# Performance work log

Measured on AMD Instinct MI355X. Metric: run time of the kernel, lower is better.

The kernel has to match this reference:

```python
import jax, jax.numpy as jnp
import numpy as np

B, S, D, H = 4, 2048, 1024, 16
DH = D // H          # per-head attention size (attention_size // n_heads)
F = 4 * D            # FFN hidden
EPS = 1e-5


def _layer_norm(x, g, b):
    m = jnp.mean(x, axis=-1, keepdims=True)
    v = jnp.mean(jnp.square(x - m), axis=-1, keepdims=True)
    return (x - m) * jax.lax.rsqrt(v + EPS) * g + b


def setup_inputs() -> dict:
    key = jax.random.key(0)
    ks = jax.random.split(key, 12)
    s = 0.02
    x = jax.random.normal(ks[0], (B, S, D), dtype=jnp.float32)
    # causal mask: True = masked (strict upper triangle)
    mask = jnp.broadcast_to(jnp.triu(jnp.ones((S, S), dtype=bool), k=1), (B, S, S))
    wq = jax.random.normal(ks[1], (H, D, DH), dtype=jnp.float32) * s
    wk = jax.random.normal(ks[2], (H, D, DH), dtype=jnp.float32) * s
    wv = jax.random.normal(ks[3], (H, D, DH), dtype=jnp.float32) * s
    wo = jax.random.normal(ks[4], (D, D), dtype=jnp.float32) * s   # attention_size -> embedding_dim
    w1 = jax.random.normal(ks[5], (D, F), dtype=jnp.float32) * s
    b1 = jax.random.normal(ks[6], (F,), dtype=jnp.float32) * s
    w2 = jax.random.normal(ks[7], (F, D), dtype=jnp.float32) * s
    b2 = jax.random.normal(ks[8], (D,), dtype=jnp.float32) * s
    ln1_g = jnp.ones((D,), jnp.float32) + jax.random.normal(ks[9], (D,), jnp.float32) * s
    ln1_b = jax.random.normal(ks[10], (D,), jnp.float32) * s
    ln2_g = jnp.ones((D,), jnp.float32) + jax.random.normal(ks[11], (D,), jnp.float32) * s
    ln2_b = jnp.zeros((D,), jnp.float32)
    return {"x": x, "mask": mask, "wq": wq, "wk": wk, "wv": wv, "wo": wo,
            "w1": w1, "b1": b1, "w2": w2, "b2": b2,
            "ln1_g": ln1_g, "ln1_b": ln1_b, "ln2_g": ln2_g, "ln2_b": ln2_b}


def reference(x, mask, wq, wk, wv, wo, w1, b1, w2, b2, ln1_g, ln1_b, ln2_g, ln2_b):
    # --- self-attention block (pre-norm, residual) ---
    h = _layer_norm(x, ln1_g, ln1_b)                       # [B,S,D]
    q = jnp.einsum('bsd,hde->bhse', h, wq)                 # [B,H,S,DH]
    k = jnp.einsum('bsd,hde->bhse', h, wk)
    v = jnp.einsum('bsd,hde->bhse', h, wv)
    scores = jnp.einsum('bhse,bhte->bhst', q, k)           # [B,H,S,S]
    # faithful to source: mask-fill with -inf, THEN divide by sqrt(head_dim)
    scores = jnp.where(mask[:, None, :, :], -jnp.inf, scores) / jnp.sqrt(jnp.float32(DH))
    p = jax.nn.softmax(scores, axis=-1)
    attn = jnp.einsum('bhst,bhte->bhse', p, v)             # [B,H,S,DH]
    concat = attn.transpose(0, 2, 1, 3).reshape(B, S, D)   # heads concatenated on feature dim
    x = x + concat @ wo
    # --- feed-forward block ---
    h2 = _layer_norm(x, ln2_g, ln2_b)
    ff = jax.nn.gelu(h2 @ w1 + b1, approximate=False) @ w2 + b2
    return x + ff
```

## Files before the change

kernel.cpp:

```cpp
#include <hip/hip_runtime.h>
#include <hip/hip_bf16.h>
#include <math.h>


#define Bz 4
#define Sz 2048
#define Dz 1024
#define Hz 16
#define DHz 64
#define Fz 4096
#define Mz 8192

typedef float f32x4 __attribute__((ext_vector_type(4)));
typedef __bf16 bf16x8 __attribute__((ext_vector_type(8)));
typedef __bf16 bf16x4 __attribute__((ext_vector_type(4)));
typedef short s16x4 __attribute__((ext_vector_type(4)));

#define GLOAD_LDS16(g, l)                                                                   \
  __builtin_amdgcn_global_load_lds((const __attribute__((address_space(1))) unsigned int*)(g), \
                                   (__attribute__((address_space(3))) unsigned int*)(l), 16, 0, 0)

static __device__ __forceinline__ unsigned short f2bu(float f) {
  unsigned int u = __float_as_uint(f);
  u += 0x7fffu + ((u >> 16) & 1u);
  return (unsigned short)(u >> 16);
}

static __device__ __forceinline__ f32x4 mfma32(bf16x8 a, bf16x8 b, f32x4 c) {
  return __builtin_amdgcn_mfma_f32_16x16x32_bf16(a, b, c, 0, 0, 0);
}
static __device__ __forceinline__ f32x4 mfma16(s16x4 a, s16x4 b, f32x4 c) {
#if __has_builtin(__builtin_amdgcn_mfma_f32_16x16x16bf16_1k)
  return __builtin_amdgcn_mfma_f32_16x16x16bf16_1k(a, b, c, 0, 0, 0);
#else
  asm("v_mfma_f32_16x16x16_bf16 %0, %1, %2, %0" : "+v"(c) : "v"(a), "v"(b));
  return c;
#endif
}

template <int OFF>
static __device__ __forceinline__ s16x4 tr16(unsigned addr) {
  s16x4 r;
  asm volatile("ds_read_b64_tr_b16 %0, %1 offset:%2" : "=v"(r) : "v"(addr), "i"(OFF));
  return r;
}


__global__ __launch_bounds__(256) void pack_qkv(
    const float* __restrict__ wq, const float* __restrict__ wk, const float* __restrict__ wv,
    unsigned short* __restrict__ outW)
{
  __shared__ float tile[64][65];
  const int blk = blockIdx.x;
  const int dc = blk & 15;
  const int h  = (blk >> 4) & 15;
  const int p  = blk >> 8;
  const float* w = p == 0 ? wq : (p == 1 ? wk : wv);
  const int tid = threadIdx.x;
#pragma unroll
  for (int i = 0; i < 4; ++i) {
    int idx = i * 256 + tid;
    int dl = idx >> 4;
    int e0 = (idx & 15) * 4;
    const float4 v = *(const float4*)&w[(size_t)(h * 1024 + dc * 64 + dl) * 64 + e0];
    tile[dl][e0 + 0] = v.x; tile[dl][e0 + 1] = v.y;
    tile[dl][e0 + 2] = v.z; tile[dl][e0 + 3] = v.w;
  }
  __syncthreads();
#pragma unroll
  for (int i = 0; i < 4; ++i) {
    int idx = i * 256 + tid;
    int e = idx >> 4;
    int d0 = (idx & 15) * 4;
    ushort4 o;
    o.x = f2bu(tile[d0 + 0][e]); o.y = f2bu(tile[d0 + 1][e]);
    o.z = f2bu(tile[d0 + 2][e]); o.w = f2bu(tile[d0 + 3][e]);
    *(ushort4*)&outW[(size_t)(p * 1024 + h * 64 + e) * 1024 + dc * 64 + d0] = o;
  }
}

__global__ __launch_bounds__(256) void transpose_f32_to_bf16(
    const float* __restrict__ in, unsigned short* __restrict__ out, int R, int C)
{
  __shared__ float tile[32][33];
  int c0 = blockIdx.x * 32, r0 = blockIdx.y * 32;
  int x = threadIdx.x, y = threadIdx.y;
#pragma unroll
  for (int i = 0; i < 32; i += 8)
    tile[y + i][x] = in[(size_t)(r0 + y + i) * C + c0 + x];
  __syncthreads();
#pragma unroll
  for (int i = 0; i < 32; i += 8)
    out[(size_t)(c0 + y + i) * R + r0 + x] = f2bu(tile[x][y + i]);
}


__global__ __launch_bounds__(256) void ln_kernel(
    const float* __restrict__ x, const float* __restrict__ gamma, const float* __restrict__ beta,
    unsigned short* __restrict__ outH)
{
  const int row = blockIdx.x;
  const int tid = threadIdx.x;
  const float4 v = ((const float4*)(x + (size_t)row * Dz))[tid];
  float s = v.x + v.y + v.z + v.w;
  float s2 = v.x * v.x + v.y * v.y + v.z * v.z + v.w * v.w;
#pragma unroll
  for (int o = 32; o > 0; o >>= 1) {
    s += __shfl_xor(s, o);
    s2 += __shfl_xor(s2, o);
  }
  __shared__ float ss[4], ss2[4];
  if ((tid & 63) == 0) { ss[tid >> 6] = s; ss2[tid >> 6] = s2; }
  __syncthreads();
  s = ss[0] + ss[1] + ss[2] + ss[3];
  s2 = ss2[0] + ss2[1] + ss2[2] + ss2[3];
  const float mean = s * (1.0f / Dz);
  const float rstd = rsqrtf(s2 * (1.0f / Dz) - mean * mean + 1e-5f);
  const float4 g4 = ((const float4*)gamma)[tid];
  const float4 b4 = ((const float4*)beta)[tid];
  ushort4 o;
  o.x = f2bu((v.x - mean) * rstd * g4.x + b4.x);
  o.y = f2bu((v.y - mean) * rstd * g4.y + b4.y);
  o.z = f2bu((v.z - mean) * rstd * g4.z + b4.z);
  o.w = f2bu((v.w - mean) * rstd * g4.w + b4.w);
  ((ushort4*)(outH + (size_t)row * Dz))[tid] = o;
}


enum { EPI_BF16 = 0, EPI_GELU_BF16 = 1, EPI_RES_F32 = 2, EPI_BIAS_RES_F32 = 3 };

template <int BM, int EPI>
__global__ __launch_bounds__(512, 2) void gemm256(
    const unsigned short* __restrict__ A,
    const unsigned short* __restrict__ BT,
    int M, int N, int K,
    const float* bias, const float* resid,
    unsigned short* outb, float* outf)
{
  constexpr int BN = 256, BK = 64;
  constexpr int DEPTH = (BM == 128) ? 3 : 2;
  constexpr int ACH = (BM * BK * 2) / (512 * 16);
  constexpr int BCH = (BN * BK * 2) / (512 * 16);
  constexpr int MREP = BM / 32;
  __shared__ unsigned short As[DEPTH][BM * BK];
  __shared__ unsigned short Bs[DEPTH][BN * BK];

  const int tid = threadIdx.x;
  const int lane = tid & 63;
  const int wid = tid >> 6;
  const int wr = wid >> 2;
  const int wc = wid & 3;
  const int rsel = lane & 15;
  const int kgrp = lane >> 4;

  const int nwg = gridDim.x;
  const int bid = blockIdx.x;
  const int id2 = (bid & 7) * (nwg >> 3) + (bid >> 3);
  const int nbx = N / BN;
  const int n0 = (id2 % nbx) * BN;
  const int m0 = (id2 / nbx) * BM;

  f32x4 acc[MREP][4] = {};

  auto issue = [&](int kt, int b) {
#pragma unroll
    for (int r = 0; r < ACH; ++r) {
      int gc = r * 512 + tid;
      int row = gc >> 3;
      int kcs = (gc & 7) ^ (row & 7);
      GLOAD_LDS16(A + (size_t)(m0 + row) * K + kt * BK + kcs * 8, &As[b][gc * 8]);
    }
#pragma unroll
    for (int r = 0; r < BCH; ++r) {
      int gc = r * 512 + tid;
      int row = gc >> 3;
      int kcs = (gc & 7) ^ (row & 7);
      GLOAD_LDS16(BT + (size_t)(n0 + row) * K + kt * BK + kcs * 8, &Bs[b][gc * 8]);
    }
  };

  const int T = K >> 6;
#pragma unroll
  for (int d = 0; d < DEPTH - 1; ++d) issue(d, d);

  for (int t = 0; t < T; ++t) {
    const int b = t % DEPTH;
    if (t + DEPTH - 1 < T) issue(t + DEPTH - 1, (t + DEPTH - 1) % DEPTH);
    int rem = T - 1 - t;
    if (rem > DEPTH - 1) rem = DEPTH - 1;
    if constexpr (DEPTH == 3) {
      if (rem == 2)      asm volatile("s_waitcnt vmcnt(12)" ::: "memory");
      else if (rem == 1) asm volatile("s_waitcnt vmcnt(6)" ::: "memory");
      else               asm volatile("s_waitcnt vmcnt(0)" ::: "memory");
    } else {
      if (rem == 1) asm volatile("s_waitcnt vmcnt(8)" ::: "memory");
      else          asm volatile("s_waitcnt vmcnt(0)" ::: "memory");
    }
    __builtin_amdgcn_sched_barrier(0);
    __builtin_amdgcn_s_barrier();
    __builtin_amdgcn_sched_barrier(0);

    const unsigned short* Ab = As[b];
    const unsigned short* Bb = Bs[b];
    __builtin_amdgcn_s_setprio(1);
#pragma unroll
    for (int kk = 0; kk < 2; ++kk) {
      bf16x8 bfr[4], af[MREP];
#pragma unroll
      for (int nf = 0; nf < 4; ++nf) {
        int br = wc * 64 + nf * 16 + rsel;
        bfr[nf] = *(const bf16x8*)&Bb[br * BK + (((kk * 4 + kgrp) ^ (br & 7)) * 8)];
      }
#pragma unroll
      for (int mf = 0; mf < MREP; ++mf) {
        int ar = wr * (BM / 2) + mf * 16 + rsel;
        af[mf] = *(const bf16x8*)&Ab[ar * BK + (((kk * 4 + kgrp) ^ (ar & 7)) * 8)];
      }
#pragma unroll
      for (int mf = 0; mf < MREP; ++mf)
#pragma unroll
        for (int nf = 0; nf < 4; ++nf)
          acc[mf][nf] = mfma32(af[mf], bfr[nf], acc[mf][nf]);
    }
    __builtin_amdgcn_s_setprio(0);
    __builtin_amdgcn_sched_barrier(0);
    __builtin_amdgcn_s_barrier();
  }

#pragma unroll
  for (int mf = 0; mf < MREP; ++mf) {
#pragma unroll
    for (int nf = 0; nf < 4; ++nf) {
      const int n = n0 + wc * 64 + nf * 16 + rsel;
#pragma unroll
      for (int j = 0; j < 4; ++j) {
        const int m = m0 + wr * (BM / 2) + mf * 16 + kgrp * 4 + j;
        const size_t idx = (size_t)m * N + n;
        float v = acc[mf][nf][j];
        if constexpr (EPI == EPI_BF16) {
          outb[idx] = f2bu(v);
        } else if constexpr (EPI == EPI_GELU_BF16) {
          v += bias[n];
          v = 0.5f * v * (1.0f + erff(v * 0.70710678118654752f));
          outb[idx] = f2bu(v);
        } else if constexpr (EPI == EPI_RES_F32) {
          outf[idx] = v + resid[idx];
        } else {
          outf[idx] = v + bias[n] + resid[idx];
        }
      }
    }
  }
}


__global__ __launch_bounds__(256, 4) void attn_kernel(
    const unsigned short* __restrict__ QKV,
    unsigned short* __restrict__ outA)
{
  __shared__ unsigned short Kt[64 * 64];
  __shared__ unsigned short Vs[64 * 64];
  const int pi = blockIdx.x;
  const int hh = blockIdx.y;
  const int bb = blockIdx.z;
  const int tid = threadIdx.x;
  const int lane = tid & 63;
  const int w = tid >> 6;
  const int rsel = lane & 15;
  const int kgrp = lane >> 4;
  const int qt[2] = {pi, 31 - pi};

  bf16x8 qf0[2], qf1[2];
  int qg[2];
#pragma unroll
  for (int s = 0; s < 2; ++s) {
    qg[s] = qt[s] * 64 + w * 16 + rsel;
    const size_t rowQ = (size_t)(bb * Sz + qg[s]) * 3072 + hh * 64;
    qf0[s] = *(const bf16x8*)&QKV[rowQ + kgrp * 8];
    qf1[s] = *(const bf16x8*)&QKV[rowQ + 32 + kgrp * 8];
  }

  f32x4 accO[2][4] = {};
  float mr[2] = {-INFINITY, -INFINITY};
  float lr[2] = {0.0f, 0.0f};

  auto vs3 = (__attribute__((address_space(3))) unsigned short*)Vs;
  const unsigned vbase = (unsigned)(uintptr_t)vs3 + (unsigned)lane * 8u;
  constexpr float SCL = 0.18033688011112042f;

  auto proc = [&](const bf16x8& q0, const bf16x8& q1, float& mrun, float& lrun,
                  f32x4* accS, s16x4* pb, bool edge, int qgs, int kb) {
    f32x4 sc[4];
    __builtin_amdgcn_s_setprio(1);
#pragma unroll
    for (int kf = 0; kf < 4; ++kf) {
      int key = kf * 16 + rsel;
      bf16x8 k0 = *(const bf16x8*)&Kt[key * 64 + ((kgrp ^ (key & 7)) * 8)];
      bf16x8 k1 = *(const bf16x8*)&Kt[key * 64 + (((4 + kgrp) ^ (key & 7)) * 8)];
      f32x4 s = {};
      s = mfma32(k0, q0, s);
      s = mfma32(k1, q1, s);
      sc[kf] = s;
    }
    __builtin_amdgcn_s_setprio(0);
    float tmax = -INFINITY;
#pragma unroll
    for (int kf = 0; kf < 4; ++kf)
#pragma unroll
      for (int j = 0; j < 4; ++j) {
        float v = sc[kf][j] * SCL;
        if (edge) {
          int keyg = kb + kf * 16 + kgrp * 4 + j;
          if (keyg > qgs) v = -INFINITY;
        }
        sc[kf][j] = v;
        tmax = fmaxf(tmax, v);
      }
    tmax = fmaxf(tmax, __shfl_xor(tmax, 16));
    tmax = fmaxf(tmax, __shfl_xor(tmax, 32));
    if (!__all(tmax <= mrun + 8.0f)) {
      const float mnew = fmaxf(mrun, tmax);
      const float corr = exp2f(mrun - mnew);
      lrun *= corr;
#pragma unroll
      for (int df = 0; df < 4; ++df) accS[df] *= corr;
      mrun = mnew;
    }
    float psum = 0.0f;
#pragma unroll
    for (int kf = 0; kf < 4; ++kf) {
      bf16x4 pv;
#pragma unroll
      for (int j = 0; j < 4; ++j) {
        float e = exp2f(sc[kf][j] - mrun);
        psum += e;
        pv[j] = (__bf16)e;
      }
      pb[kf] = __builtin_bit_cast(s16x4, pv);
    }
    psum += __shfl_xor(psum, 16);
    psum += __shfl_xor(psum, 32);
    lrun += psum;
  };

  for (int kt = 0; kt <= qt[1]; ++kt) {
    const int kb = kt * 64;
    if (kt) __syncthreads();
#pragma unroll
    for (int r = 0; r < 2; ++r) {
      int c = r * 256 + tid;
      int key = c >> 3;
      int dcs = (c & 7) ^ (key & 7);
      GLOAD_LDS16(QKV + (size_t)(bb * Sz + kb + key) * 3072 + 1024 + hh * 64 + dcs * 8,
                  &Kt[c * 8]);
    }
#pragma unroll
    for (int r = 0; r < 2; ++r) {
      int c = r * 256 + tid;
      int key = ((c >> 3) & 15) * 4 + ((c >> 1) & 3);
      int d = (c >> 7) * 16 + (c & 1) * 8;
      GLOAD_LDS16(QKV + (size_t)(bb * Sz + kb + key) * 3072 + 2048 + hh * 64 + d,
                  &Vs[c * 8]);
    }
    __syncthreads();

    s16x4 pb[2][4];
#pragma unroll
    for (int s = 0; s < 2; ++s)
      if (kt <= qt[s])
        proc(qf0[s], qf1[s], mr[s], lr[s], accO[s], pb[s], kt == qt[s], qg[s], kb);

#pragma unroll
    for (int df = 0; df < 4; ++df) {
      unsigned a = vbase + df * 2048;
      s16x4 vf0 = tr16<0>(a);
      s16x4 vf1 = tr16<512>(a);
      s16x4 vf2 = tr16<1024>(a);
      s16x4 vf3 = tr16<1536>(a);
      asm volatile("s_waitcnt lgkmcnt(0)" ::: "memory");
      __builtin_amdgcn_sched_barrier(0);
      __builtin_amdgcn_s_setprio(1);
#pragma unroll
      for (int s = 0; s < 2; ++s) {
        if (kt <= qt[s]) {
          accO[s][df] = mfma16(vf0, pb[s][0], accO[s][df]);
          accO[s][df] = mfma16(vf1, pb[s][1], accO[s][df]);
          accO[s][df] = mfma16(vf2, pb[s][2], accO[s][df]);
          accO[s][df] = mfma16(vf3, pb[s][3], accO[s][df]);
        }
      }
      __builtin_amdgcn_s_setprio(0);
    }
  }

#pragma unroll
  for (int s = 0; s < 2; ++s) {
    const float rl = 1.0f / lr[s];
    const size_t orow = (size_t)(bb * Sz + qg[s]) * Dz + hh * 64;
#pragma unroll
    for (int df = 0; df < 4; ++df) {
      s16x4 o;
#pragma unroll
      for (int j = 0; j < 4; ++j) o[j] = (short)f2bu(accO[s][df][j] * rl);
      *(s16x4*)&outA[orow + df * 16 + kgrp * 4] = o;
    }
  }
}


extern "C" void kernel_launch(void* const* d_in, const int* in_sizes, int n_in,
                              void* d_out, int out_size, void* d_ws, size_t ws_size,
                              hipStream_t stream) {
  const float* x   = (const float*)d_in[0];
  const float* wq  = (const float*)d_in[2];
  const float* wk  = (const float*)d_in[3];
  const float* wv  = (const float*)d_in[4];
  const float* wo  = (const float*)d_in[5];
  const float* w1  = (const float*)d_in[6];
  const float* b1  = (const float*)d_in[7];
  const float* w2  = (const float*)d_in[8];
  const float* b2  = (const float*)d_in[9];
  const float* g1  = (const float*)d_in[10];
  const float* be1 = (const float*)d_in[11];
  const float* g2  = (const float*)d_in[12];
  const float* be2 = (const float*)d_in[13];
  float* out = (float*)d_out;

  char* ws = (char*)d_ws;
  unsigned short* WqkvT = (unsigned short*)(ws);
  unsigned short* WoT   = (unsigned short*)(ws + 6291456);
  unsigned short* W1T   = (unsigned short*)(ws + 8388608);
  unsigned short* W2T   = (unsigned short*)(ws + 16777216);
  unsigned short* hbuf  = (unsigned short*)(ws + 25165824);
  unsigned short* big   = (unsigned short*)(ws + 41943040);

  dim3 tb(32, 8);
  pack_qkv<<<768, 256, 0, stream>>>(wq, wk, wv, WqkvT);
  transpose_f32_to_bf16<<<dim3(32, 32), tb, 0, stream>>>(wo, WoT, 1024, 1024);
  transpose_f32_to_bf16<<<dim3(128, 32), tb, 0, stream>>>(w1, W1T, 1024, 4096);
  transpose_f32_to_bf16<<<dim3(32, 128), tb, 0, stream>>>(w2, W2T, 4096, 1024);

  ln_kernel<<<Mz, 256, 0, stream>>>(x, g1, be1, hbuf);
  gemm256<128, EPI_BF16><<<768, 512, 0, stream>>>(
      hbuf, WqkvT, Mz, 3072, 1024, nullptr, nullptr, big, nullptr);
  attn_kernel<<<dim3(16, 16, 4), 256, 0, stream>>>(big, hbuf);
  gemm256<128, EPI_RES_F32><<<256, 512, 0, stream>>>(
      hbuf, WoT, Mz, 1024, 1024, nullptr, x, nullptr, out);
  ln_kernel<<<Mz, 256, 0, stream>>>(out, g2, be2, hbuf);
  gemm256<256, EPI_GELU_BF16><<<512, 512, 0, stream>>>(
      hbuf, W1T, Mz, Fz, 1024, b1, nullptr, big, nullptr);
  gemm256<128, EPI_BIAS_RES_F32><<<256, 512, 0, stream>>>(
      big, W2T, Mz, 1024, Fz, b2, out, nullptr, out);
}
```

Measured before the change: 441.2 us.

## Remap GEMM tiles into per-XCD 4x4 groups and use 128-row tiles everywhere

Replaces the simple XCD round-robin block swizzle with a grouped mapping. Each XCD gets a contiguous band of M rows, and blocks within it walk 4x4 tile chunks so neighbouring blocks share A and B panels in the XCD-local L2. It also drops the BM=256 variant used for the FFN1 GEMM, so every GEMM uses 128x256 tiles with a 3-deep pipeline, and the FFN1 grid doubles to 1024 blocks. The mapping assumes the row and column tile counts divide evenly into 4-wide groups per XCD, which holds for these shapes.

```diff
diff --git a/kernel.cpp b/kernel.cpp
--- a/kernel.cpp
+++ b/kernel.cpp
@@ -129,7 +129,7 @@
 
 enum { EPI_BF16 = 0, EPI_GELU_BF16 = 1, EPI_RES_F32 = 2, EPI_BIAS_RES_F32 = 3 };
 
-template <int BM, int EPI>
+template <int EPI>
 __global__ __launch_bounds__(512, 2) void gemm256(
     const unsigned short* __restrict__ A,
     const unsigned short* __restrict__ BT,
@@ -137,11 +137,9 @@
     const float* bias, const float* resid,
     unsigned short* outb, float* outf)
 {
-  constexpr int BN = 256, BK = 64;
-  constexpr int DEPTH = (BM == 128) ? 3 : 2;
-  constexpr int ACH = (BM * BK * 2) / (512 * 16);
-  constexpr int BCH = (BN * BK * 2) / (512 * 16);
-  constexpr int MREP = BM / 32;
+  constexpr int BM = 128, BN = 256, BK = 64, DEPTH = 3;
+  constexpr int ACH = 2, BCH = 4;
+  constexpr int MREP = 4;
   __shared__ unsigned short As[DEPTH][BM * BK];
   __shared__ unsigned short Bs[DEPTH][BN * BK];
 
@@ -153,12 +151,15 @@
   const int rsel = lane & 15;
   const int kgrp = lane >> 4;
 
-  const int nwg = gridDim.x;
-  const int bid = blockIdx.x;
-  const int id2 = (bid & 7) * (nwg >> 3) + (bid >> 3);
   const int nbx = N / BN;
-  const int n0 = (id2 % nbx) * BN;
-  const int m0 = (id2 / nbx) * BM;
+  const int xcd = blockIdx.x & 7;
+  const int l = blockIdx.x >> 3;
+  const int ncw = nbx >> 2;
+  const int chunk = l >> 4, sub = l & 15;
+  const int mch = chunk / ncw, nch = chunk % ncw;
+  const int rowsPerXcd = (gridDim.x >> 3) / nbx;
+  const int m0 = (xcd * rowsPerXcd + mch * 4 + (sub >> 2)) * BM;
+  const int n0 = (nch * 4 + (sub & 3)) * BN;
 
   f32x4 acc[MREP][4] = {};
 
@@ -180,22 +181,16 @@
   };
 
   const int T = K >> 6;
-#pragma unroll
-  for (int d = 0; d < DEPTH - 1; ++d) issue(d, d);
+  issue(0, 0); issue(1, 1);
 
   for (int t = 0; t < T; ++t) {
     const int b = t % DEPTH;
-    if (t + DEPTH - 1 < T) issue(t + DEPTH - 1, (t + DEPTH - 1) % DEPTH);
+    if (t + 2 < T) issue(t + 2, (t + 2) % DEPTH);
     int rem = T - 1 - t;
-    if (rem > DEPTH - 1) rem = DEPTH - 1;
-    if constexpr (DEPTH == 3) {
-      if (rem == 2)      asm volatile("s_waitcnt vmcnt(12)" ::: "memory");
-      else if (rem == 1) asm volatile("s_waitcnt vmcnt(6)" ::: "memory");
-      else               asm volatile("s_waitcnt vmcnt(0)" ::: "memory");
-    } else {
-      if (rem == 1) asm volatile("s_waitcnt vmcnt(8)" ::: "memory");
-      else          asm volatile("s_waitcnt vmcnt(0)" ::: "memory");
-    }
+    if (rem > 2) rem = 2;
+    if (rem == 2)      asm volatile("s_waitcnt vmcnt(12)" ::: "memory");
+    else if (rem == 1) asm volatile("s_waitcnt vmcnt(6)" ::: "memory");
+    else               asm volatile("s_waitcnt vmcnt(0)" ::: "memory");
     __builtin_amdgcn_sched_barrier(0);
     __builtin_amdgcn_s_barrier();
     __builtin_amdgcn_sched_barrier(0);
@@ -213,7 +208,7 @@
       }
 #pragma unroll
       for (int mf = 0; mf < MREP; ++mf) {
-        int ar = wr * (BM / 2) + mf * 16 + rsel;
+        int ar = wr * 64 + mf * 16 + rsel;
         af[mf] = *(const bf16x8*)&Ab[ar * BK + (((kk * 4 + kgrp) ^ (ar & 7)) * 8)];
       }
 #pragma unroll
@@ -234,7 +229,7 @@
       const int n = n0 + wc * 64 + nf * 16 + rsel;
 #pragma unroll
       for (int j = 0; j < 4; ++j) {
-        const int m = m0 + wr * (BM / 2) + mf * 16 + kgrp * 4 + j;
+        const int m = m0 + wr * 64 + mf * 16 + kgrp * 4 + j;
         const size_t idx = (size_t)m * N + n;
         float v = acc[mf][nf][j];
         if constexpr (EPI == EPI_BF16) {
@@ -441,14 +436,14 @@
   transpose_f32_to_bf16<<<dim3(32, 128), tb, 0, stream>>>(w2, W2T, 4096, 1024);
 
   ln_kernel<<<Mz, 256, 0, stream>>>(x, g1, be1, hbuf);
-  gemm256<128, EPI_BF16><<<768, 512, 0, stream>>>(
+  gemm256<EPI_BF16><<<768, 512, 0, stream>>>(
       hbuf, WqkvT, Mz, 3072, 1024, nullptr, nullptr, big, nullptr);
   attn_kernel<<<dim3(16, 16, 4), 256, 0, stream>>>(big, hbuf);
-  gemm256<128, EPI_RES_F32><<<256, 512, 0, stream>>>(
+  gemm256<EPI_RES_F32><<<256, 512, 0, stream>>>(
       hbuf, WoT, Mz, 1024, 1024, nullptr, x, nullptr, out);
   ln_kernel<<<Mz, 256, 0, stream>>>(out, g2, be2, hbuf);
-  gemm256<256, EPI_GELU_BF16><<<512, 512, 0, stream>>>(
+  gemm256<EPI_GELU_BF16><<<1024, 512, 0, stream>>>(
       hbuf, W1T, Mz, Fz, 1024, b1, nullptr, big, nullptr);
-  gemm256<128, EPI_BIAS_RES_F32><<<256, 512, 0, stream>>>(
+  gemm256<EPI_BIAS_RES_F32><<<256, 512, 0, stream>>>(
       big, W2T, Mz, 1024, Fz, b2, out, nullptr, out);
 }
```

New measurement: 462.9 us. +4.9%, slower.

## Double-buffer K/V tiles in attention kernel to overlap loads with compute

Applied to the files above, without the earlier changes.

The attention kernel now keeps two LDS buffers for K and V. It issues the global-to-LDS loads for the next key tile before computing on the current one, and waits with a partial vmcnt so only the current tile's loads must complete. This aims to hide global memory latency behind the MFMA and softmax work. In exchange it doubles LDS use, which may lower occupancy under the 4-block launch bound, and it relies on hand-counted vmcnt values and explicit barriers being correct.

```diff
diff --git a/kernel.cpp b/kernel.cpp
--- a/kernel.cpp
+++ b/kernel.cpp
@@ -258,8 +258,8 @@
     const unsigned short* __restrict__ QKV,
     unsigned short* __restrict__ outA)
 {
-  __shared__ unsigned short Kt[64 * 64];
-  __shared__ unsigned short Vs[64 * 64];
+  __shared__ unsigned short Kt[2][64 * 64];
+  __shared__ unsigned short Vs[2][64 * 64];
   const int pi = blockIdx.x;
   const int hh = blockIdx.y;
   const int bb = blockIdx.z;
@@ -284,19 +284,40 @@
   float mr[2] = {-INFINITY, -INFINITY};
   float lr[2] = {0.0f, 0.0f};
 
-  auto vs3 = (__attribute__((address_space(3))) unsigned short*)Vs;
+  auto vs3 = (__attribute__((address_space(3))) unsigned short*)&Vs[0][0];
   const unsigned vbase = (unsigned)(uintptr_t)vs3 + (unsigned)lane * 8u;
   constexpr float SCL = 0.18033688011112042f;
 
-  auto proc = [&](const bf16x8& q0, const bf16x8& q1, float& mrun, float& lrun,
-                  f32x4* accS, s16x4* pb, bool edge, int qgs, int kb) {
+  auto stage = [&](int kt, int b) {
+    const int kb = kt * 64;
+#pragma unroll
+    for (int r = 0; r < 2; ++r) {
+      int c = r * 256 + tid;
+      int key = c >> 3;
+      int dcs = (c & 7) ^ (key & 7);
+      GLOAD_LDS16(QKV + (size_t)(bb * Sz + kb + key) * 3072 + 1024 + hh * 64 + dcs * 8,
+                  &Kt[b][c * 8]);
+    }
+#pragma unroll
+    for (int r = 0; r < 2; ++r) {
+      int c = r * 256 + tid;
+      int key = ((c >> 3) & 15) * 4 + ((c >> 1) & 3);
+      int d = (c >> 7) * 16 + (c & 1) * 8;
+      GLOAD_LDS16(QKV + (size_t)(bb * Sz + kb + key) * 3072 + 2048 + hh * 64 + d,
+                  &Vs[b][c * 8]);
+    }
+  };
+
+  auto proc = [&](const unsigned short* Kb, const bf16x8& q0, const bf16x8& q1,
+                  float& mrun, float& lrun, f32x4* accS, s16x4* pb,
+                  bool edge, int qgs, int kb) {
     f32x4 sc[4];
     __builtin_amdgcn_s_setprio(1);
 #pragma unroll
     for (int kf = 0; kf < 4; ++kf) {
       int key = kf * 16 + rsel;
-      bf16x8 k0 = *(const bf16x8*)&Kt[key * 64 + ((kgrp ^ (key & 7)) * 8)];
-      bf16x8 k1 = *(const bf16x8*)&Kt[key * 64 + (((4 + kgrp) ^ (key & 7)) * 8)];
+      bf16x8 k0 = *(const bf16x8*)&Kb[key * 64 + ((kgrp ^ (key & 7)) * 8)];
+      bf16x8 k1 = *(const bf16x8*)&Kb[key * 64 + (((4 + kgrp) ^ (key & 7)) * 8)];
       f32x4 s = {};
       s = mfma32(k0, q0, s);
       s = mfma32(k1, q1, s);
@@ -343,36 +364,32 @@
     lrun += psum;
   };
 
+  stage(0, 0);
+
   for (int kt = 0; kt <= qt[1]; ++kt) {
     const int kb = kt * 64;
-    if (kt) __syncthreads();
-#pragma unroll
-    for (int r = 0; r < 2; ++r) {
-      int c = r * 256 + tid;
-      int key = c >> 3;
-      int dcs = (c & 7) ^ (key & 7);
-      GLOAD_LDS16(QKV + (size_t)(bb * Sz + kb + key) * 3072 + 1024 + hh * 64 + dcs * 8,
-                  &Kt[c * 8]);
-    }
-#pragma unroll
-    for (int r = 0; r < 2; ++r) {
-      int c = r * 256 + tid;
-      int key = ((c >> 3) & 15) * 4 + ((c >> 1) & 3);
-      int d = (c >> 7) * 16 + (c & 1) * 8;
-      GLOAD_LDS16(QKV + (size_t)(bb * Sz + kb + key) * 3072 + 2048 + hh * 64 + d,
-                  &Vs[c * 8]);
-    }
-    __syncthreads();
+    const int cur = kt & 1;
+    if (kt < qt[1]) {
+      stage(kt + 1, cur ^ 1);
+      asm volatile("s_waitcnt vmcnt(4)" ::: "memory");
+    } else {
+      asm volatile("s_waitcnt vmcnt(0)" ::: "memory");
+    }
+    __builtin_amdgcn_sched_barrier(0);
+    __builtin_amdgcn_s_barrier();
+    __builtin_amdgcn_sched_barrier(0);
 
     s16x4 pb[2][4];
 #pragma unroll
     for (int s = 0; s < 2; ++s)
       if (kt <= qt[s])
-        proc(qf0[s], qf1[s], mr[s], lr[s], accO[s], pb[s], kt == qt[s], qg[s], kb);
-
+        proc(Kt[cur], qf0[s], qf1[s], mr[s], lr[s], accO[s], pb[s],
+             kt == qt[s], qg[s], kb);
+
+    const unsigned vb = vbase + (unsigned)cur * 8192u;
 #pragma unroll
     for (int df = 0; df < 4; ++df) {
-      unsigned a = vbase + df * 2048;
+      unsigned a = vb + df * 2048;
       s16x4 vf0 = tr16<0>(a);
       s16x4 vf1 = tr16<512>(a);
       s16x4 vf2 = tr16<1024>(a);
@@ -391,6 +408,9 @@
       }
       __builtin_amdgcn_s_setprio(0);
     }
+
+    __builtin_amdgcn_sched_barrier(0);
+    __builtin_amdgcn_s_barrier();
   }
 
 #pragma unroll
```

New measurement: 453.8 us. +2.8%, slower.
